# Kernel tuning notes

Measured on AMD Instinct MI355X. Metric: run time of the kernel, lower is better.

## Reference

```python
import jax, jax.numpy as jnp
import numpy as np

BETA = 1e10  # hard softmax temperature from the original module


def setup_inputs() -> dict:
    key = jax.random.key(0)
    ks = jax.random.split(key, 7)
    bs, nc, units, feat = 128, 1024, 512, 512
    return {
        "x": jax.random.normal(ks[0], (bs, feat), jnp.float32),
        "class_logits": jax.random.normal(ks[1], (bs, nc), jnp.float32),
        "h_states": jax.random.normal(ks[2], (nc, units), jnp.float32) * 0.1,
        "c_states": jax.random.normal(ks[3], (nc, units), jnp.float32) * 0.1,
        "kernel": jax.random.normal(ks[4], (feat, 4 * units), jnp.float32) * 0.05,
        "rec_kernel": jax.random.normal(ks[5], (units, 4 * units), jnp.float32) * 0.05,
        "bias": jnp.zeros((4 * units,), jnp.float32),
    }


def _diff_scatter(A, B, w):
    # A: (nc, u) old class states, B: (bs, u) new states, w: (bs, nc) hard softmax.
    # Faithful to tf version: broadcast to (nc, bs, u), blend, then reduce_max over bs.
    m = w.T[:, :, None]                       # (nc, bs, 1)
    blended = A[:, None, :] * (1.0 - m) + B[None, :, :] * m  # (nc, bs, u)
    return jnp.max(blended, axis=1)           # (nc, u)


def reference(x, class_logits, h_states, c_states, kernel, rec_kernel, bias):
    # diff_gather: softmax-weighted sum over classes == weights @ params
    w = jax.nn.softmax(class_logits * BETA, axis=-1)  # (bs, nc), ~one-hot
    h0 = w @ h_states                                  # (bs, u)
    c0 = w @ c_states                                  # (bs, u)

    # single-step Keras LSTM (seq_len == 1): gate order i, f, c, o
    z = x @ kernel + h0 @ rec_kernel + bias            # (bs, 4u)
    i, f, g, o = jnp.split(z, 4, axis=-1)
    i = jax.nn.sigmoid(i)
    f = jax.nn.sigmoid(f)
    g = jnp.tanh(g)
    o = jax.nn.sigmoid(o)
    c = f * c0 + i * g
    h = o * jnp.tanh(c)                                # LSTM output == h

    new_h = _diff_scatter(h_states, h, w)
    new_c = _diff_scatter(c_states, c, w)
    return h, new_h, new_c
```

## Files before the change

kernel.cpp:

```cpp
#include <hip/hip_runtime.h>
#include <hip/hip_bf16.h>
#include <math.h>

#define BS    128
#define NC    1024
#define UNITS 512
#define FEAT  512
#define FOURU 2048
#define KG    8
#define NT    32
#define WPAD  40

typedef short  bf16x8 __attribute__((ext_vector_type(8)));
typedef float  f32x4  __attribute__((ext_vector_type(4)));

__device__ __forceinline__ unsigned short bf_rhu(float f) {
    union { float f; unsigned u; } v; v.f = f;
    return (unsigned short)((v.u + 0x8000u) >> 16);
}
__device__ __forceinline__ unsigned pack2(float a, float b) {
    return (unsigned)bf_rhu(a) | ((unsigned)bf_rhu(b) << 16);
}

__global__ __launch_bounds__(256) void argmax_prep_kernel(
    const float* __restrict__ logits, const float* __restrict__ x,
    const float* __restrict__ h_states,
    int* __restrict__ sidx, unsigned* __restrict__ Abf )
{
    int b = blockIdx.x;
    int t = threadIdx.x;
    float best = -INFINITY; int bi = 0;
    for (int i = t; i < NC; i += 256) {
        float v = logits[b * NC + i];
        if (v > best) { best = v; bi = i; }
    }
    for (int off = 32; off > 0; off >>= 1) {
        float ov = __shfl_down(best, off);
        int   oi = __shfl_down(bi, off);
        if (ov > best || (ov == best && oi < bi)) { best = ov; bi = oi; }
    }
    __shared__ float sv[4]; __shared__ int si[4];
    __shared__ int sbi;
    int wid = t >> 6;
    if ((t & 63) == 0) { sv[wid] = best; si[wid] = bi; }
    __syncthreads();
    if (t == 0) {
        for (int w = 1; w < 4; ++w)
            if (sv[w] > best || (sv[w] == best && si[w] < bi)) { best = sv[w]; bi = si[w]; }
        sidx[b] = bi;
        sbi = bi;
    }
    __syncthreads();
    int st = t & 127;
    const float* srcrow = (t < 128) ? (x + (long)b * FEAT)
                                    : (h_states + (long)sbi * UNITS);
    float4 v = *(const float4*)(srcrow + st * 4);
    unsigned lo = pack2(v.x, v.y), hi = pack2(v.z, v.w);
    unsigned du = (unsigned)b * 512u + (t < 128 ? 0u : 256u) + (unsigned)st * 2u;
    *(uint2*)(Abf + du) = make_uint2(lo, hi);
}

__global__ __launch_bounds__(256) void gemm_kernel(
    const unsigned short* __restrict__ Abf,
    const float* __restrict__ kern, const float* __restrict__ reck,
    float* __restrict__ z_part)
{
    __shared__ __align__(16) unsigned short as[BS * 32];
    __shared__ __align__(16) unsigned short wst[NT * WPAD];

    int t = threadIdx.x;
    int ntile = blockIdx.x * NT;
    int kg = blockIdx.y;
    const float* W = (kg < 4) ? kern : reck;
    int wk0base = (kg & 3) * 128;
    int k0base  = kg * 128;

    int wid = t >> 6, lane = t & 63;
    int l15 = lane & 15, quad = lane >> 4;

    f32x4 zero = {0.f, 0.f, 0.f, 0.f};
    f32x4 acc[2][2] = {{zero, zero}, {zero, zero}};

    for (int kstep = 0; kstep < 4; ++kstep) {
        int k0  = k0base  + kstep * 32;
        int wk0 = wk0base + kstep * 32;

        for (int r = 0; r < 2; ++r) {
            int G = r * 256 + t;
            int m = G >> 2;
            int p = G & 3;
            int c = (p ^ (m >> 1)) & 3;
            bf16x8 v = *(const bf16x8*)(Abf + (long)m * 1024 + k0 + c * 8);
            *(bf16x8*)&as[G * 8] = v;
        }
        for (int p = 0; p < 4; ++p) {
            int kk = (t >> 5) + p * 8;
            int n  = t & 31;
            wst[n * WPAD + kk] = bf_rhu(W[(long)(wk0 + kk) * FOURU + ntile + n]);
        }
        __syncthreads();

        bf16x8 afrag[2], bfrag[2];
        for (int ms = 0; ms < 2; ++ms) {
            int m = wid * 32 + ms * 16 + l15;
            afrag[ms] = *(const bf16x8*)&as[(m * 4 + ((quad ^ (m >> 1)) & 3)) * 8];
        }
        for (int ns = 0; ns < 2; ++ns) {
            int n = ns * 16 + l15;
            bfrag[ns] = *(const bf16x8*)&wst[n * WPAD + quad * 8];
        }
        for (int ms = 0; ms < 2; ++ms)
            for (int ns = 0; ns < 2; ++ns)
                acc[ms][ns] = __builtin_amdgcn_mfma_f32_16x16x32_bf16(
                                  afrag[ms], bfrag[ns], acc[ms][ns], 0, 0, 0);
        __syncthreads();
    }

    float* zp = z_part + (long)kg * BS * FOURU;
    for (int ms = 0; ms < 2; ++ms)
        for (int ns = 0; ns < 2; ++ns)
            for (int r = 0; r < 4; ++r) {
                int m = wid * 32 + ms * 16 + quad * 4 + r;
                int n = ntile + ns * 16 + l15;
                zp[(long)m * FOURU + n] = acc[ms][ns][r];
            }
}

__global__ __launch_bounds__(256) void scatter_lstm_kernel(
    const float* __restrict__ z_part, const float* __restrict__ bias,
    const float* __restrict__ h_states, const float* __restrict__ c_states,
    const int* __restrict__ sidx,
    float* __restrict__ h_out, float* __restrict__ out_h, float* __restrict__ out_c)
{
    __shared__ int s[BS];
    int t = threadIdx.x;
    if (t < BS) s[t] = sidx[t];
    __syncthreads();
    int j = blockIdx.x >> 1;
    int u = (blockIdx.x & 1) * 256 + t;

    float ah = h_states[(long)j * UNITS + u];
    float ac = c_states[(long)j * UNITS + u];

    float mh = -INFINITY, mc = -INFINITY;
    int count = 0;
    float bi_ = bias[u], bf_ = bias[512 + u], bg_ = bias[1024 + u], bo_ = bias[1536 + u];

    for (int b = 0; b < BS; ++b) {
        if (s[b] == j) {
            ++count;
            float zi = bi_, zf = bf_, zg = bg_, zo = bo_;
            #pragma unroll
            for (int kg = 0; kg < KG; ++kg) {
                const float* zp = z_part + (long)kg * BS * FOURU + (long)b * FOURU;
                zi += zp[u];
                zf += zp[512 + u];
                zg += zp[1024 + u];
                zo += zp[1536 + u];
            }
            float ig = 1.f / (1.f + expf(-zi));
            float fg = 1.f / (1.f + expf(-zf));
            float gg = tanhf(zg);
            float og = 1.f / (1.f + expf(-zo));
            float c  = fg * ac + ig * gg;
            float h  = og * tanhf(c);
            h_out[(long)b * UNITS + u] = h;
            mh = fmaxf(mh, h);
            mc = fmaxf(mc, c);
        }
    }
    out_h[(long)j * UNITS + u] = (count == BS) ? mh : fmaxf(ah, mh);
    out_c[(long)j * UNITS + u] = (count == BS) ? mc : fmaxf(ac, mc);
}

extern "C" void kernel_launch(void* const* d_in, const int* in_sizes, int n_in,
                              void* d_out, int out_size, void* d_ws, size_t ws_size,
                              hipStream_t stream)
{
    (void)in_sizes; (void)n_in; (void)out_size; (void)ws_size;
    const float* x      = (const float*)d_in[0];
    const float* logits = (const float*)d_in[1];
    const float* h_st   = (const float*)d_in[2];
    const float* c_st   = (const float*)d_in[3];
    const float* kern   = (const float*)d_in[4];
    const float* reck   = (const float*)d_in[5];
    const float* bias   = (const float*)d_in[6];

    float* out        = (float*)d_out;
    float* out_h_step = out;
    float* out_newh   = out + BS * UNITS;
    float* out_newc   = out + BS * UNITS + NC * UNITS;

    char*     ws     = (char*)d_ws;
    int*      sidx   = (int*)ws;
    unsigned* Abf    = (unsigned*)(ws + 1024);
    float*    z_part = (float*)(ws + 1024 * 1024);

    argmax_prep_kernel<<<BS, 256, 0, stream>>>(logits, x, h_st, sidx, Abf);
    gemm_kernel<<<dim3(FOURU / NT, KG), 256, 0, stream>>>(
        (const unsigned short*)Abf, kern, reck, z_part);
    scatter_lstm_kernel<<<NC * UNITS / 256, 256, 0, stream>>>(
        z_part, bias, h_st, c_st, sidx, out_h_step, out_newh, out_newc);
}
```

Baseline: 105.8 us.

## Fuse argmax, GEMM, and scatter-LSTM into one persistent kernel with grid barriers

```diff
diff --git a/kernel.cpp b/kernel.cpp
--- a/kernel.cpp
+++ b/kernel.cpp
@@ -8,11 +8,10 @@
 #define FEAT  512
 #define FOURU 2048
 #define KG    8
-#define NT    32
-#define WPAD  40
-
-typedef short  bf16x8 __attribute__((ext_vector_type(8)));
-typedef float  f32x4  __attribute__((ext_vector_type(4)));
+#define NBLK  512
+
+typedef short bf16x8 __attribute__((ext_vector_type(8)));
+typedef float f32x4  __attribute__((ext_vector_type(4)));
 
 __device__ __forceinline__ unsigned short bf_rhu(float f) {
     union { float f; unsigned u; } v; v.f = f;
@@ -22,155 +21,165 @@
     return (unsigned)bf_rhu(a) | ((unsigned)bf_rhu(b) << 16);
 }
 
-__global__ __launch_bounds__(256) void argmax_prep_kernel(
-    const float* __restrict__ logits, const float* __restrict__ x,
-    const float* __restrict__ h_states,
-    int* __restrict__ sidx, unsigned* __restrict__ Abf )
-{
-    int b = blockIdx.x;
-    int t = threadIdx.x;
-    float best = -INFINITY; int bi = 0;
-    for (int i = t; i < NC; i += 256) {
-        float v = logits[b * NC + i];
-        if (v > best) { best = v; bi = i; }
-    }
-    for (int off = 32; off > 0; off >>= 1) {
-        float ov = __shfl_down(best, off);
-        int   oi = __shfl_down(bi, off);
-        if (ov > best || (ov == best && oi < bi)) { best = ov; bi = oi; }
-    }
-    __shared__ float sv[4]; __shared__ int si[4];
-    __shared__ int sbi;
-    int wid = t >> 6;
-    if ((t & 63) == 0) { sv[wid] = best; si[wid] = bi; }
+__device__ __forceinline__ void gbar(unsigned* cnt, unsigned target) {
     __syncthreads();
-    if (t == 0) {
-        for (int w = 1; w < 4; ++w)
-            if (sv[w] > best || (sv[w] == best && si[w] < bi)) { best = sv[w]; bi = si[w]; }
-        sidx[b] = bi;
-        sbi = bi;
+    if (threadIdx.x == 0) {
+        __threadfence();
+        __hip_atomic_fetch_add(cnt, 1u, __ATOMIC_ACQ_REL, __HIP_MEMORY_SCOPE_AGENT);
+        while (__hip_atomic_load(cnt, __ATOMIC_ACQUIRE, __HIP_MEMORY_SCOPE_AGENT) < target)
+            __builtin_amdgcn_s_sleep(8);
+        __threadfence();
     }
     __syncthreads();
-    int st = t & 127;
-    const float* srcrow = (t < 128) ? (x + (long)b * FEAT)
-                                    : (h_states + (long)sbi * UNITS);
-    float4 v = *(const float4*)(srcrow + st * 4);
-    unsigned lo = pack2(v.x, v.y), hi = pack2(v.z, v.w);
-    unsigned du = (unsigned)b * 512u + (t < 128 ? 0u : 256u) + (unsigned)st * 2u;
-    *(uint2*)(Abf + du) = make_uint2(lo, hi);
-}
-
-__global__ __launch_bounds__(256) void gemm_kernel(
-    const unsigned short* __restrict__ Abf,
+}
+
+__global__ __launch_bounds__(256, 2) void fused_kernel(
+    const float* __restrict__ x, const float* __restrict__ logits,
+    const float* __restrict__ h_st, const float* __restrict__ c_st,
     const float* __restrict__ kern, const float* __restrict__ reck,
-    float* __restrict__ z_part)
-{
-    __shared__ __align__(16) unsigned short as[BS * 32];
-    __shared__ __align__(16) unsigned short wst[NT * WPAD];
-
-    int t = threadIdx.x;
-    int ntile = blockIdx.x * NT;
-    int kg = blockIdx.y;
-    const float* W = (kg < 4) ? kern : reck;
-    int wk0base = (kg & 3) * 128;
-    int k0base  = kg * 128;
-
-    int wid = t >> 6, lane = t & 63;
-    int l15 = lane & 15, quad = lane >> 4;
-
-    f32x4 zero = {0.f, 0.f, 0.f, 0.f};
-    f32x4 acc[2][2] = {{zero, zero}, {zero, zero}};
-
-    for (int kstep = 0; kstep < 4; ++kstep) {
-        int k0  = k0base  + kstep * 32;
-        int wk0 = wk0base + kstep * 32;
-
-        for (int r = 0; r < 2; ++r) {
-            int G = r * 256 + t;
-            int m = G >> 2;
-            int p = G & 3;
-            int c = (p ^ (m >> 1)) & 3;
-            bf16x8 v = *(const bf16x8*)(Abf + (long)m * 1024 + k0 + c * 8);
-            *(bf16x8*)&as[G * 8] = v;
-        }
-        for (int p = 0; p < 4; ++p) {
-            int kk = (t >> 5) + p * 8;
-            int n  = t & 31;
-            wst[n * WPAD + kk] = bf_rhu(W[(long)(wk0 + kk) * FOURU + ntile + n]);
-        }
-        __syncthreads();
-
-        bf16x8 afrag[2], bfrag[2];
-        for (int ms = 0; ms < 2; ++ms) {
-            int m = wid * 32 + ms * 16 + l15;
-            afrag[ms] = *(const bf16x8*)&as[(m * 4 + ((quad ^ (m >> 1)) & 3)) * 8];
-        }
-        for (int ns = 0; ns < 2; ++ns) {
-            int n = ns * 16 + l15;
-            bfrag[ns] = *(const bf16x8*)&wst[n * WPAD + quad * 8];
-        }
-        for (int ms = 0; ms < 2; ++ms)
-            for (int ns = 0; ns < 2; ++ns)
-                acc[ms][ns] = __builtin_amdgcn_mfma_f32_16x16x32_bf16(
-                                  afrag[ms], bfrag[ns], acc[ms][ns], 0, 0, 0);
-        __syncthreads();
-    }
-
-    float* zp = z_part + (long)kg * BS * FOURU;
-    for (int ms = 0; ms < 2; ++ms)
-        for (int ns = 0; ns < 2; ++ns)
-            for (int r = 0; r < 4; ++r) {
-                int m = wid * 32 + ms * 16 + quad * 4 + r;
-                int n = ntile + ns * 16 + l15;
-                zp[(long)m * FOURU + n] = acc[ms][ns][r];
-            }
-}
-
-__global__ __launch_bounds__(256) void scatter_lstm_kernel(
-    const float* __restrict__ z_part, const float* __restrict__ bias,
-    const float* __restrict__ h_states, const float* __restrict__ c_states,
-    const int* __restrict__ sidx,
+    const float* __restrict__ bias,
+    unsigned* __restrict__ bar, int* __restrict__ sidx,
+    unsigned short* __restrict__ Abf,
+    unsigned short* __restrict__ Wt,
+    float* __restrict__ z_part,
     float* __restrict__ h_out, float* __restrict__ out_h, float* __restrict__ out_c)
 {
-    __shared__ int s[BS];
-    int t = threadIdx.x;
+    const int bid = blockIdx.x, t = threadIdx.x;
+    const int wid = t >> 6, lane = t & 63, l15 = lane & 15, quad = lane >> 4;
+
+    __shared__ int   s[BS];
+    __shared__ float sv[4];
+    __shared__ int   si[4];
+    __shared__ int   sbi;
+
+    if (bid < BS) {
+        int b = bid;
+        float best = -INFINITY; int bi = 0;
+        for (int i = t; i < NC; i += 256) {
+            float v = logits[b * NC + i];
+            if (v > best) { best = v; bi = i; }
+        }
+        for (int off = 32; off > 0; off >>= 1) {
+            float ov = __shfl_down(best, off);
+            int   oi = __shfl_down(bi, off);
+            if (ov > best || (ov == best && oi < bi)) { best = ov; bi = oi; }
+        }
+        if ((t & 63) == 0) { sv[wid] = best; si[wid] = bi; }
+        __syncthreads();
+        if (t == 0) {
+            for (int w = 1; w < 4; ++w)
+                if (sv[w] > best || (sv[w] == best && si[w] < bi)) { best = sv[w]; bi = si[w]; }
+            sidx[b] = bi;
+            sbi = bi;
+        }
+        __syncthreads();
+        int st = t & 127;
+        const float* srcrow = (t < 128) ? (x + (long)b * FEAT)
+                                        : (h_st + (long)sbi * UNITS);
+        float4 v = *(const float4*)(srcrow + st * 4);
+        unsigned lo = pack2(v.x, v.y), hi = pack2(v.z, v.w);
+        unsigned du = (unsigned)b * 512u + (t < 128 ? 0u : 256u) + (unsigned)st * 2u;
+        *(uint2*)((unsigned*)Abf + du) = make_uint2(lo, hi);
+    } else {
+        int gw = (bid - BS) * 4 + wid;
+        for (int task = gw; task < 4096; task += 1536) {
+            int kc = task >> 5;
+            int n  = (task & 31) * 64 + lane;
+            int r0 = kc * 8;
+            const float* base = (r0 < 512) ? (kern + (long)r0 * FOURU + n)
+                                           : (reck + (long)(r0 - 512) * FOURU + n);
+            bf16x8 o;
+            #pragma unroll
+            for (int j = 0; j < 8; ++j)
+                o[j] = (short)bf_rhu(base[(long)j * FOURU]);
+            *(bf16x8*)(Wt + (long)n * 1024 + r0) = o;
+        }
+    }
+    gbar(bar, NBLK);
+
+    {
+        int nt = bid & 63, kg = bid >> 6;
+        int k0base = kg * 128 + quad * 8;
+        f32x4 zero = {0.f, 0.f, 0.f, 0.f};
+        f32x4 acc[2][2] = {{zero, zero}, {zero, zero}};
+        #pragma unroll
+        for (int kstep = 0; kstep < 4; ++kstep) {
+            int k0 = k0base + kstep * 32;
+            bf16x8 af[2], wf[2];
+            #pragma unroll
+            for (int ms = 0; ms < 2; ++ms) {
+                int m = wid * 32 + ms * 16 + l15;
+                af[ms] = *(const bf16x8*)(Abf + (long)m * 1024 + k0);
+            }
+            #pragma unroll
+            for (int ns = 0; ns < 2; ++ns) {
+                int n = nt * 32 + ns * 16 + l15;
+                wf[ns] = *(const bf16x8*)(Wt + (long)n * 1024 + k0);
+            }
+            #pragma unroll
+            for (int ms = 0; ms < 2; ++ms)
+                #pragma unroll
+                for (int ns = 0; ns < 2; ++ns)
+                    acc[ms][ns] = __builtin_amdgcn_mfma_f32_16x16x32_bf16(
+                                      af[ms], wf[ns], acc[ms][ns], 0, 0, 0);
+        }
+        float* zp = z_part + (long)kg * BS * FOURU;
+        #pragma unroll
+        for (int ms = 0; ms < 2; ++ms)
+            #pragma unroll
+            for (int ns = 0; ns < 2; ++ns)
+                #pragma unroll
+                for (int r = 0; r < 4; ++r) {
+                    int m = wid * 32 + ms * 16 + quad * 4 + r;
+                    int n = nt * 32 + ns * 16 + l15;
+                    zp[(long)m * FOURU + n] = acc[ms][ns][r];
+                }
+    }
+    gbar(bar + 1, NBLK);
+
     if (t < BS) s[t] = sidx[t];
     __syncthreads();
-    int j = blockIdx.x >> 1;
-    int u = (blockIdx.x & 1) * 256 + t;
-
-    float ah = h_states[(long)j * UNITS + u];
-    float ac = c_states[(long)j * UNITS + u];
-
-    float mh = -INFINITY, mc = -INFINITY;
-    int count = 0;
-    float bi_ = bias[u], bf_ = bias[512 + u], bg_ = bias[1024 + u], bo_ = bias[1536 + u];
-
-    for (int b = 0; b < BS; ++b) {
-        if (s[b] == j) {
-            ++count;
-            float zi = bi_, zf = bf_, zg = bg_, zo = bo_;
-            #pragma unroll
-            for (int kg = 0; kg < KG; ++kg) {
-                const float* zp = z_part + (long)kg * BS * FOURU + (long)b * FOURU;
-                zi += zp[u];
-                zf += zp[512 + u];
-                zg += zp[1024 + u];
-                zo += zp[1536 + u];
+    float bi0 = bias[t],        bi1 = bias[256 + t];
+    float bf0 = bias[512 + t],  bf1 = bias[768 + t];
+    float bg0 = bias[1024 + t], bg1 = bias[1280 + t];
+    float bo0 = bias[1536 + t], bo1 = bias[1792 + t];
+
+    for (int jj = 0; jj < 2; ++jj) {
+        int j = bid * 2 + jj;
+        float ah0 = h_st[(long)j * UNITS + t], ah1 = h_st[(long)j * UNITS + 256 + t];
+        float ac0 = c_st[(long)j * UNITS + t], ac1 = c_st[(long)j * UNITS + 256 + t];
+        float mh0 = -INFINITY, mh1 = -INFINITY, mc0 = -INFINITY, mc1 = -INFINITY;
+        int cnt = 0;
+        for (int b = 0; b < BS; ++b) {
+            if (s[b] == j) {
+                ++cnt;
+                float zi0 = bi0, zi1 = bi1, zf0 = bf0, zf1 = bf1;
+                float zg0 = bg0, zg1 = bg1, zo0 = bo0, zo1 = bo1;
+                #pragma unroll
+                for (int g = 0; g < KG; ++g) {
+                    const float* z = z_part + (long)g * BS * FOURU + (long)b * FOURU;
+                    zi0 += z[t];        zi1 += z[256 + t];
+                    zf0 += z[512 + t];  zf1 += z[768 + t];
+                    zg0 += z[1024 + t]; zg1 += z[1280 + t];
+                    zo0 += z[1536 + t]; zo1 += z[1792 + t];
+                }
+                float i0 = 1.f/(1.f+expf(-zi0)), i1 = 1.f/(1.f+expf(-zi1));
+                float f0 = 1.f/(1.f+expf(-zf0)), f1 = 1.f/(1.f+expf(-zf1));
+                float g0 = tanhf(zg0),           g1 = tanhf(zg1);
+                float o0 = 1.f/(1.f+expf(-zo0)), o1 = 1.f/(1.f+expf(-zo1));
+                float c0 = f0*ac0 + i0*g0,       c1 = f1*ac1 + i1*g1;
+                float h0 = o0*tanhf(c0),         h1 = o1*tanhf(c1);
+                h_out[(long)b * UNITS + t]       = h0;
+                h_out[(long)b * UNITS + 256 + t] = h1;
+                mh0 = fmaxf(mh0, h0); mh1 = fmaxf(mh1, h1);
+                mc0 = fmaxf(mc0, c0); mc1 = fmaxf(mc1, c1);
             }
-            float ig = 1.f / (1.f + expf(-zi));
-            float fg = 1.f / (1.f + expf(-zf));
-            float gg = tanhf(zg);
-            float og = 1.f / (1.f + expf(-zo));
-            float c  = fg * ac + ig * gg;
-            float h  = og * tanhf(c);
-            h_out[(long)b * UNITS + u] = h;
-            mh = fmaxf(mh, h);
-            mc = fmaxf(mc, c);
-        }
-    }
-    out_h[(long)j * UNITS + u] = (count == BS) ? mh : fmaxf(ah, mh);
-    out_c[(long)j * UNITS + u] = (count == BS) ? mc : fmaxf(ac, mc);
+        }
+        out_h[(long)j * UNITS + t]       = (cnt == BS) ? mh0 : fmaxf(ah0, mh0);
+        out_h[(long)j * UNITS + 256 + t] = (cnt == BS) ? mh1 : fmaxf(ah1, mh1);
+        out_c[(long)j * UNITS + t]       = (cnt == BS) ? mc0 : fmaxf(ac0, mc0);
+        out_c[(long)j * UNITS + 256 + t] = (cnt == BS) ? mc1 : fmaxf(ac1, mc1);
+    }
 }
 
 extern "C" void kernel_launch(void* const* d_in, const int* in_sizes, int n_in,
@@ -191,14 +200,15 @@
     float* out_newh   = out + BS * UNITS;
     float* out_newc   = out + BS * UNITS + NC * UNITS;
 
-    char*     ws     = (char*)d_ws;
-    int*      sidx   = (int*)ws;
-    unsigned* Abf    = (unsigned*)(ws + 1024);
-    float*    z_part = (float*)(ws + 1024 * 1024);
-
-    argmax_prep_kernel<<<BS, 256, 0, stream>>>(logits, x, h_st, sidx, Abf);
-    gemm_kernel<<<dim3(FOURU / NT, KG), 256, 0, stream>>>(
-        (const unsigned short*)Abf, kern, reck, z_part);
-    scatter_lstm_kernel<<<NC * UNITS / 256, 256, 0, stream>>>(
-        z_part, bias, h_st, c_st, sidx, out_h_step, out_newh, out_newc);
-}
+    char*           ws     = (char*)d_ws;
+    unsigned*       bar    = (unsigned*)ws;
+    int*            sidx   = (int*)(ws + 256);
+    unsigned short* Abf    = (unsigned short*)(ws + 4096);
+    float*          z_part = (float*)(ws + (1u << 20));
+    unsigned short* Wt     = (unsigned short*)(ws + 10u * (1u << 20));
+
+    hipMemsetAsync(bar, 0, 2 * sizeof(unsigned), stream);
+    fused_kernel<<<NBLK, 256, 0, stream>>>(x, logits, h_st, c_st, kern, reck, bias,
+                                           bar, sidx, Abf, Wt, z_part,
+                                           out_h_step, out_newh, out_newc);
+}
```

After: 241.7 us. +128.5%, slower.
